# Optimization experiments

Hardware: AMD Instinct MI355X
Metric: run time of the kernel (lower is better)

The kernel has to match this reference:

```python
import jax, jax.numpy as jnp
import numpy as np

# icosphere level 6
NV = 40962   # vertices
NF = 81920   # faces
B = 16
CIN = 32
COUT = 32
NCOEFF = 4


def _spmm(rows, cols, vals, nrows, x):
    """Sparse (COO) @ dense over the vertex/face axis.
    x: [B, C, N] -> out: [B, C, nrows].
    """
    # gather columns, scale by nonzero values, scatter-add into rows
    g = x.transpose(2, 0, 1)[cols] * vals[:, None, None]   # [nnz, B, C]
    out = jax.ops.segment_sum(g, rows, num_segments=nrows)  # [nrows, B, C]
    return out.transpose(1, 2, 0)                           # [B, C, nrows]


def setup_inputs() -> dict:
    key = jax.random.key(0)
    ks = jax.random.split(key, 10)
    x = jax.random.normal(ks[0], (B, CIN, NV), dtype=jnp.float32)

    # G: [3*NF, NV], 3 nnz per row (3 vertices per face), component-major rows
    g_nnz = 3 * NF * 3
    G_rows = jnp.repeat(jnp.arange(3 * NF, dtype=jnp.int32), 3)
    G_cols = jax.random.randint(ks[1], (g_nnz,), 0, NV, dtype=jnp.int32)
    G_vals = jax.random.normal(ks[2], (g_nnz,), dtype=jnp.float32) * 0.5

    # L: [NV, NV], ~7 nnz per row (vertex valence + self)
    l_nnz = NV * 7
    L_rows = jnp.repeat(jnp.arange(NV, dtype=jnp.int32), 7)
    L_cols = jax.random.randint(ks[3], (l_nnz,), 0, NV, dtype=jnp.int32)
    L_vals = jax.random.normal(ks[4], (l_nnz,), dtype=jnp.float32) * 0.5

    # F2V: [NV, NF], ~6 faces per vertex, averaging weights
    f_nnz = NV * 6
    F2V_rows = jnp.repeat(jnp.arange(NV, dtype=jnp.int32), 6)
    F2V_cols = jax.random.randint(ks[5], (f_nnz,), 0, NF, dtype=jnp.int32)
    F2V_vals = jnp.full((f_nnz,), 1.0 / 6.0, dtype=jnp.float32)

    # per-face east-west / north-south tangent vectors: [NF, 3]
    EW = jax.random.normal(ks[6], (NF, 3), dtype=jnp.float32)
    NS = jax.random.normal(ks[7], (NF, 3), dtype=jnp.float32)

    stdv = 1.0 / np.sqrt(CIN * NCOEFF)
    coeffs = jax.random.uniform(ks[8], (COUT, CIN, NCOEFF), dtype=jnp.float32,
                                minval=-stdv, maxval=stdv)
    bias = jax.random.uniform(ks[9], (COUT,), dtype=jnp.float32,
                              minval=-stdv, maxval=stdv)

    return {
        "x": x,
        "G_rows": G_rows, "G_cols": G_cols, "G_vals": G_vals,
        "L_rows": L_rows, "L_cols": L_cols, "L_vals": L_vals,
        "F2V_rows": F2V_rows, "F2V_cols": F2V_cols, "F2V_vals": F2V_vals,
        "EW": EW, "NS": NS,
        "coeffs": coeffs, "bias": bias,
    }


def reference(x, G_rows, G_cols, G_vals, L_rows, L_cols, L_vals,
              F2V_rows, F2V_cols, F2V_vals, EW, NS, coeffs, bias):
    b, c, nv = x.shape
    # gradient on faces: [B,C,3*NF] -> [B,C,3,NF] -> [B,C,NF,3]
    grad_face = _spmm(G_rows, G_cols, G_vals, 3 * NF, x)
    grad_face = grad_face.reshape(b, c, 3, NF).transpose(0, 1, 3, 2)
    # Laplacian on vertices (stride=1 -> nv_prev = nv)
    laplacian = _spmm(L_rows, L_cols, L_vals, NV, x)
    identity = x  # x[..., :nv_prev] with nv_prev == nv
    # project face gradients onto EW / NS frames
    grad_face_ew = jnp.sum(grad_face * EW, axis=-1)  # [B,C,NF]
    grad_face_ns = jnp.sum(grad_face * NS, axis=-1)
    # average back to vertices
    grad_vert_ew = _spmm(F2V_rows, F2V_cols, F2V_vals, NV, grad_face_ew)
    grad_vert_ns = _spmm(F2V_rows, F2V_cols, F2V_vals, NV, grad_face_ns)
    # combine 4 features with learned per-channel coefficients
    feat = jnp.stack([identity, laplacian, grad_vert_ew, grad_vert_ns], axis=-1)  # [B,C,NV,4]
    out = jnp.einsum('bcnk,ock->bon', feat, coeffs) + bias[:, None]
    return out
```

## Files before the change

kernel.cpp:

```cpp
#include <hip/hip_runtime.h>
#include <hip/hip_bf16.h>

#define NVERT 40962
#define NFACE 81920
#define GRID_V ((NVERT + 3) / 4)
#define GRID_F (NFACE / 4)

typedef unsigned int uint;
typedef __attribute__((ext_vector_type(4))) uint  uintx4;
typedef __attribute__((ext_vector_type(4))) float floatx4;
typedef __attribute__((ext_vector_type(8))) short shortx8;

__device__ __forceinline__ uint packbf2(float a, float b) {
  uint ua = __float_as_uint(a); ua = ua + 0x7fffu + ((ua >> 16) & 1u);
  uint ub = __float_as_uint(b); ub = ub + 0x7fffu + ((ub >> 16) & 1u);
  return (ua >> 16) | (ub & 0xffff0000u);
}
__device__ __forceinline__ float2 unpackbf2(uint u) {
  float2 r;
  r.x = __uint_as_float(u << 16);
  r.y = __uint_as_float(u & 0xffff0000u);
  return r;
}
__device__ __forceinline__ short bfr(float x) {
  uint u = __float_as_uint(x);
  u = u + 0x7fffu + ((u >> 16) & 1u);
  return (short)(u >> 16);
}

__device__ __forceinline__ int swz(int blk, int nwg) {
  int q = nwg >> 3, r = nwg & 7;
  int xcd = blk & 7, idx = blk >> 3;
  return (xcd < r ? xcd * (q + 1) : r * (q + 1) + (xcd - r) * q) + idx;
}

__global__ __launch_bounds__(256) void k_transpose(const float* __restrict__ x,
                                                   uint* __restrict__ xT) {
  __shared__ float tile[32][33];
  int n0 = blockIdx.x * 32;
  int r0 = blockIdx.y * 32;
  int tx = threadIdx.x & 31;
  int ty = threadIdx.x >> 5;
#pragma unroll
  for (int i = 0; i < 32; i += 8) {
    int n = n0 + tx;
    tile[ty + i][tx] = (n < NVERT) ? x[(size_t)(r0 + ty + i) * NVERT + n] : 0.f;
  }
  __syncthreads();
#pragma unroll
  for (int i = 0; i < 32; i += 16) {
    int nl = (threadIdx.x >> 4) + i;
    int u  = threadIdx.x & 15;
    int n  = n0 + nl;
    int ug = 16 * blockIdx.y + u;
    int up = (ug & 3) * 64 + (ug >> 4) * 4 + ((ug >> 2) & 3);
    if (n < NVERT)
      xT[(size_t)n * 256 + up] = packbf2(tile[2 * u][nl], tile[2 * u + 1][nl]);
  }
}

__global__ __launch_bounds__(256) void k_faces(
    const uint* __restrict__ xT,
    const int* __restrict__ Gc, const float* __restrict__ Gv,
    const float* __restrict__ EW, const float* __restrict__ NS,
    uint* __restrict__ gf) {
  const int t = threadIdx.x, lane = t & 63, wid = t >> 6;
  int f = swz(blockIdx.x, GRID_F) * 4 + wid;

  float gr[3][4][2];
#pragma unroll
  for (int c = 0; c < 3; ++c)
#pragma unroll
    for (int ks = 0; ks < 4; ++ks) { gr[c][ks][0] = 0.f; gr[c][ks][1] = 0.f; }

#pragma unroll
  for (int comp = 0; comp < 3; ++comp) {
    int base = comp * (3 * NFACE) + 3 * f;
#pragma unroll
    for (int j = 0; j < 3; ++j) {
      int col = Gc[base + j];
      float v = Gv[base + j];
      uintx4 g = *(const uintx4*)(xT + (size_t)col * 256 + 4 * lane);
#pragma unroll
      for (int ks = 0; ks < 4; ++ks) {
        float2 p = unpackbf2(g[ks]);
        gr[comp][ks][0] = fmaf(v, p.x, gr[comp][ks][0]);
        gr[comp][ks][1] = fmaf(v, p.y, gr[comp][ks][1]);
      }
    }
  }
  float e0 = EW[3 * f], e1 = EW[3 * f + 1], e2 = EW[3 * f + 2];
  float s0 = NS[3 * f], s1 = NS[3 * f + 1], s2 = NS[3 * f + 2];
  uintx4 we, wn;
#pragma unroll
  for (int ks = 0; ks < 4; ++ks) {
    float ex = fmaf(e2, gr[2][ks][0], fmaf(e1, gr[1][ks][0], e0 * gr[0][ks][0]));
    float ey = fmaf(e2, gr[2][ks][1], fmaf(e1, gr[1][ks][1], e0 * gr[0][ks][1]));
    float sx = fmaf(s2, gr[2][ks][0], fmaf(s1, gr[1][ks][0], s0 * gr[0][ks][0]));
    float sy = fmaf(s2, gr[2][ks][1], fmaf(s1, gr[1][ks][1], s0 * gr[0][ks][1]));
    we[ks] = packbf2(ex, ey);
    wn[ks] = packbf2(sx, sy);
  }
  uint* op = gf + (size_t)f * 512 + 4 * lane;
  *(uintx4*)op         = we;
  *(uintx4*)(op + 256) = wn;
}

__global__ __launch_bounds__(256) void k_verts(
    const uint* __restrict__ xT,
    const int* __restrict__ Lc, const float* __restrict__ Lv,
    const int* __restrict__ Fc, const float* __restrict__ Fv,
    const uint* __restrict__ gf,
    const float* __restrict__ coeffs, const float* __restrict__ bias,
    float* __restrict__ out) {
  const int t = threadIdx.x, lane = t & 63, wid = t >> 6;
  int n = swz(blockIdx.x, GRID_V) * 4 + wid;
  if (n >= NVERT) return;
  const int h = lane >> 4, bm = lane & 15;

  uintx4 idw = *(const uintx4*)(xT + (size_t)n * 256 + 4 * lane);

  float lap[4][2], ewa[4][2], nsa[4][2];
#pragma unroll
  for (int ks = 0; ks < 4; ++ks) {
    lap[ks][0] = 0.f; lap[ks][1] = 0.f;
    ewa[ks][0] = 0.f; ewa[ks][1] = 0.f;
    nsa[ks][0] = 0.f; nsa[ks][1] = 0.f;
  }

#pragma unroll
  for (int j = 0; j < 7; ++j) {
    int col = Lc[7 * n + j];
    float v = Lv[7 * n + j];
    uintx4 g = *(const uintx4*)(xT + (size_t)col * 256 + 4 * lane);
#pragma unroll
    for (int ks = 0; ks < 4; ++ks) {
      float2 p = unpackbf2(g[ks]);
      lap[ks][0] = fmaf(v, p.x, lap[ks][0]);
      lap[ks][1] = fmaf(v, p.y, lap[ks][1]);
    }
  }
#pragma unroll
  for (int j = 0; j < 6; ++j) {
    int fc = Fc[6 * n + j];
    float v = Fv[6 * n + j];
    const uint* rp = gf + (size_t)fc * 512 + 4 * lane;
    uintx4 ge = *(const uintx4*)rp;
    uintx4 gn = *(const uintx4*)(rp + 256);
#pragma unroll
    for (int ks = 0; ks < 4; ++ks) {
      float2 a = unpackbf2(ge[ks]);
      float2 b = unpackbf2(gn[ks]);
      ewa[ks][0] = fmaf(v, a.x, ewa[ks][0]); ewa[ks][1] = fmaf(v, a.y, ewa[ks][1]);
      nsa[ks][0] = fmaf(v, b.x, nsa[ks][0]); nsa[ks][1] = fmaf(v, b.y, nsa[ks][1]);
    }
  }

  shortx8 afr[4];
#pragma unroll
  for (int ks = 0; ks < 4; ++ks) {
    float2 ip = unpackbf2(idw[ks]);
    shortx8 a;
    a[0] = bfr(ip.x);       a[1] = bfr(lap[ks][0]);
    a[2] = bfr(ewa[ks][0]); a[3] = bfr(nsa[ks][0]);
    a[4] = bfr(ip.y);       a[5] = bfr(lap[ks][1]);
    a[6] = bfr(ewa[ks][1]); a[7] = bfr(nsa[ks][1]);
    afr[ks] = a;
  }

  float b0 = bias[bm], b1 = bias[16 + bm];
  floatx4 acc0 = {b0, b0, b0, b0};
  floatx4 acc1 = {b1, b1, b1, b1};

#pragma unroll
  for (int ks = 0; ks < 4; ++ks) {
    const float* wp0 = coeffs + (size_t)bm * 128 + 32 * ks + 8 * h;
    floatx4 w0 = *(const floatx4*)wp0;
    floatx4 w1 = *(const floatx4*)(wp0 + 4);
    shortx8 bf0;
    bf0[0] = bfr(w0[0]); bf0[1] = bfr(w0[1]); bf0[2] = bfr(w0[2]); bf0[3] = bfr(w0[3]);
    bf0[4] = bfr(w1[0]); bf0[5] = bfr(w1[1]); bf0[6] = bfr(w1[2]); bf0[7] = bfr(w1[3]);
    acc0 = __builtin_amdgcn_mfma_f32_16x16x32_bf16(afr[ks], bf0, acc0, 0, 0, 0);

    const float* wp1 = wp0 + 16 * 128;
    floatx4 w2 = *(const floatx4*)wp1;
    floatx4 w3 = *(const floatx4*)(wp1 + 4);
    shortx8 bf1;
    bf1[0] = bfr(w2[0]); bf1[1] = bfr(w2[1]); bf1[2] = bfr(w2[2]); bf1[3] = bfr(w2[3]);
    bf1[4] = bfr(w3[0]); bf1[5] = bfr(w3[1]); bf1[6] = bfr(w3[2]); bf1[7] = bfr(w3[3]);
    acc1 = __builtin_amdgcn_mfma_f32_16x16x32_bf16(afr[ks], bf1, acc1, 0, 0, 0);
  }

#pragma unroll
  for (int reg = 0; reg < 4; ++reg) {
    int b = h * 4 + reg;
    out[(size_t)(b * 32 + bm) * NVERT + n]      = acc0[reg];
    out[(size_t)(b * 32 + 16 + bm) * NVERT + n] = acc1[reg];
  }
}

extern "C" void kernel_launch(void* const* d_in, const int* in_sizes, int n_in,
                              void* d_out, int out_size, void* d_ws, size_t ws_size,
                              hipStream_t stream) {
  const float* x      = (const float*)d_in[0];
  const int*   Gc     = (const int*)  d_in[2];
  const float* Gv     = (const float*)d_in[3];
  const int*   Lc     = (const int*)  d_in[5];
  const float* Lv     = (const float*)d_in[6];
  const int*   Fc     = (const int*)  d_in[8];
  const float* Fv     = (const float*)d_in[9];
  const float* EW     = (const float*)d_in[10];
  const float* NS     = (const float*)d_in[11];
  const float* coeffs = (const float*)d_in[12];
  const float* bias   = (const float*)d_in[13];
  float* out = (float*)d_out;

  uint* xT = (uint*)d_ws;
  uint* gf = xT + (size_t)NVERT * 256;

  dim3 gT((NVERT + 31) / 32, 16);
  k_transpose<<<gT, 256, 0, stream>>>(x, xT);
  k_faces<<<GRID_F, 256, 0, stream>>>(xT, Gc, Gv, EW, NS, gf);
  k_verts<<<GRID_V, 256, 0, stream>>>(xT, Lc, Lv, Fc, Fv, gf, coeffs, bias, out);
}
```

Baseline: 513.2 us.

## Fold tangent projection into face gather, precompute bf16 weights, raise occupancy

The face kernel now multiplies each gradient value by the EW/NS components as it gathers, keeping 16 accumulators instead of 24 and dropping the separate projection step. A small new kernel converts the coefficients to bf16 MFMA fragments once, so the vertex kernel loads them directly instead of converting per wave. Launch bounds now request 8 blocks per CU, and the face/vertex index is made wave-uniform with readfirstlane so index loads can be scalar. This adds one tiny kernel launch and may cause register spills under the tighter occupancy bound.

Result: slower. 978.8 us (+90.7%).

```diff
diff --git a/kernel.cpp b/kernel.cpp
--- a/kernel.cpp
+++ b/kernel.cpp
@@ -59,80 +59,91 @@
   }
 }
 
-__global__ __launch_bounds__(256) void k_faces(
+__global__ __launch_bounds__(256) void k_prepw(const float* __restrict__ coeffs,
+                                               short* __restrict__ wsW) {
+  int t = threadIdx.x;
+  int ks = t >> 6, lane = t & 63;
+  int bm = lane & 15, h = lane >> 4;
+  const float* wp0 = coeffs + (size_t)bm * 128 + 32 * ks + 8 * h;
+  shortx8 f0, f1;
+#pragma unroll
+  for (int j = 0; j < 8; ++j) {
+    f0[j] = bfr(wp0[j]);
+    f1[j] = bfr(wp0[16 * 128 + j]);
+  }
+  *(shortx8*)(wsW + ((size_t)(ks * 2 + 0) * 64 + lane) * 8) = f0;
+  *(shortx8*)(wsW + ((size_t)(ks * 2 + 1) * 64 + lane) * 8) = f1;
+}
+
+__global__ __launch_bounds__(256, 8) void k_faces(
     const uint* __restrict__ xT,
     const int* __restrict__ Gc, const float* __restrict__ Gv,
     const float* __restrict__ EW, const float* __restrict__ NS,
     uint* __restrict__ gf) {
-  const int t = threadIdx.x, lane = t & 63, wid = t >> 6;
-  int f = swz(blockIdx.x, GRID_F) * 4 + wid;
-
-  float gr[3][4][2];
-#pragma unroll
-  for (int c = 0; c < 3; ++c)
-#pragma unroll
-    for (int ks = 0; ks < 4; ++ks) { gr[c][ks][0] = 0.f; gr[c][ks][1] = 0.f; }
+  const int t = threadIdx.x, lane = t & 63;
+  const int f = __builtin_amdgcn_readfirstlane(swz(blockIdx.x, GRID_F) * 4 + (t >> 6));
+  const int voff = 4 * lane;
+
+  float ea[4][2], sa[4][2];
+#pragma unroll
+  for (int ks = 0; ks < 4; ++ks) {
+    ea[ks][0] = 0.f; ea[ks][1] = 0.f;
+    sa[ks][0] = 0.f; sa[ks][1] = 0.f;
+  }
 
 #pragma unroll
   for (int comp = 0; comp < 3; ++comp) {
-    int base = comp * (3 * NFACE) + 3 * f;
+    const int base = comp * (3 * NFACE) + 3 * f;
+    const float ewc = EW[3 * f + comp];
+    const float nsc = NS[3 * f + comp];
 #pragma unroll
     for (int j = 0; j < 3; ++j) {
-      int col = Gc[base + j];
-      float v = Gv[base + j];
-      uintx4 g = *(const uintx4*)(xT + (size_t)col * 256 + 4 * lane);
+      const int col = Gc[base + j];
+      const float v = Gv[base + j];
+      const float ve = v * ewc, vn = v * nsc;
+      uintx4 g = *(const uintx4*)(xT + (size_t)col * 256 + voff);
 #pragma unroll
       for (int ks = 0; ks < 4; ++ks) {
         float2 p = unpackbf2(g[ks]);
-        gr[comp][ks][0] = fmaf(v, p.x, gr[comp][ks][0]);
-        gr[comp][ks][1] = fmaf(v, p.y, gr[comp][ks][1]);
+        ea[ks][0] = fmaf(ve, p.x, ea[ks][0]); ea[ks][1] = fmaf(ve, p.y, ea[ks][1]);
+        sa[ks][0] = fmaf(vn, p.x, sa[ks][0]); sa[ks][1] = fmaf(vn, p.y, sa[ks][1]);
       }
     }
   }
-  float e0 = EW[3 * f], e1 = EW[3 * f + 1], e2 = EW[3 * f + 2];
-  float s0 = NS[3 * f], s1 = NS[3 * f + 1], s2 = NS[3 * f + 2];
   uintx4 we, wn;
 #pragma unroll
   for (int ks = 0; ks < 4; ++ks) {
-    float ex = fmaf(e2, gr[2][ks][0], fmaf(e1, gr[1][ks][0], e0 * gr[0][ks][0]));
-    float ey = fmaf(e2, gr[2][ks][1], fmaf(e1, gr[1][ks][1], e0 * gr[0][ks][1]));
-    float sx = fmaf(s2, gr[2][ks][0], fmaf(s1, gr[1][ks][0], s0 * gr[0][ks][0]));
-    float sy = fmaf(s2, gr[2][ks][1], fmaf(s1, gr[1][ks][1], s0 * gr[0][ks][1]));
-    we[ks] = packbf2(ex, ey);
-    wn[ks] = packbf2(sx, sy);
-  }
-  uint* op = gf + (size_t)f * 512 + 4 * lane;
+    we[ks] = packbf2(ea[ks][0], ea[ks][1]);
+    wn[ks] = packbf2(sa[ks][0], sa[ks][1]);
+  }
+  uint* op = gf + (size_t)f * 512 + voff;
   *(uintx4*)op         = we;
   *(uintx4*)(op + 256) = wn;
 }
 
-__global__ __launch_bounds__(256) void k_verts(
+__global__ __launch_bounds__(256, 8) void k_verts(
     const uint* __restrict__ xT,
     const int* __restrict__ Lc, const float* __restrict__ Lv,
     const int* __restrict__ Fc, const float* __restrict__ Fv,
     const uint* __restrict__ gf,
-    const float* __restrict__ coeffs, const float* __restrict__ bias,
+    const short* __restrict__ wsW, const float* __restrict__ bias,
     float* __restrict__ out) {
-  const int t = threadIdx.x, lane = t & 63, wid = t >> 6;
-  int n = swz(blockIdx.x, GRID_V) * 4 + wid;
+  const int t = threadIdx.x, lane = t & 63;
+  const int n = __builtin_amdgcn_readfirstlane(swz(blockIdx.x, GRID_V) * 4 + (t >> 6));
   if (n >= NVERT) return;
   const int h = lane >> 4, bm = lane & 15;
-
-  uintx4 idw = *(const uintx4*)(xT + (size_t)n * 256 + 4 * lane);
-
-  float lap[4][2], ewa[4][2], nsa[4][2];
-#pragma unroll
-  for (int ks = 0; ks < 4; ++ks) {
-    lap[ks][0] = 0.f; lap[ks][1] = 0.f;
-    ewa[ks][0] = 0.f; ewa[ks][1] = 0.f;
-    nsa[ks][0] = 0.f; nsa[ks][1] = 0.f;
-  }
-
+  const int voff = 4 * lane;
+
+  uintx4 idw = *(const uintx4*)(xT + (size_t)n * 256 + voff);
+
+  float lap[4][2];
+#pragma unroll
+  for (int ks = 0; ks < 4; ++ks) { lap[ks][0] = 0.f; lap[ks][1] = 0.f; }
 #pragma unroll
   for (int j = 0; j < 7; ++j) {
-    int col = Lc[7 * n + j];
-    float v = Lv[7 * n + j];
-    uintx4 g = *(const uintx4*)(xT + (size_t)col * 256 + 4 * lane);
+    const int col = Lc[7 * n + j];
+    const float v = Lv[7 * n + j];
+    uintx4 g = *(const uintx4*)(xT + (size_t)col * 256 + voff);
 #pragma unroll
     for (int ks = 0; ks < 4; ++ks) {
       float2 p = unpackbf2(g[ks]);
@@ -140,19 +151,26 @@
       lap[ks][1] = fmaf(v, p.y, lap[ks][1]);
     }
   }
+
+  float ea[4][2], na[4][2];
+#pragma unroll
+  for (int ks = 0; ks < 4; ++ks) {
+    ea[ks][0] = 0.f; ea[ks][1] = 0.f;
+    na[ks][0] = 0.f; na[ks][1] = 0.f;
+  }
 #pragma unroll
   for (int j = 0; j < 6; ++j) {
-    int fc = Fc[6 * n + j];
-    float v = Fv[6 * n + j];
-    const uint* rp = gf + (size_t)fc * 512 + 4 * lane;
+    const int fc = Fc[6 * n + j];
+    const float v = Fv[6 * n + j];
+    const uint* rp = gf + (size_t)fc * 512 + voff;
     uintx4 ge = *(const uintx4*)rp;
     uintx4 gn = *(const uintx4*)(rp + 256);
 #pragma unroll
     for (int ks = 0; ks < 4; ++ks) {
       float2 a = unpackbf2(ge[ks]);
       float2 b = unpackbf2(gn[ks]);
-      ewa[ks][0] = fmaf(v, a.x, ewa[ks][0]); ewa[ks][1] = fmaf(v, a.y, ewa[ks][1]);
-      nsa[ks][0] = fmaf(v, b.x, nsa[ks][0]); nsa[ks][1] = fmaf(v, b.y, nsa[ks][1]);
+      ea[ks][0] = fmaf(v, a.x, ea[ks][0]); ea[ks][1] = fmaf(v, a.y, ea[ks][1]);
+      na[ks][0] = fmaf(v, b.x, na[ks][0]); na[ks][1] = fmaf(v, b.y, na[ks][1]);
     }
   }
 
@@ -161,33 +179,21 @@
   for (int ks = 0; ks < 4; ++ks) {
     float2 ip = unpackbf2(idw[ks]);
     shortx8 a;
-    a[0] = bfr(ip.x);       a[1] = bfr(lap[ks][0]);
-    a[2] = bfr(ewa[ks][0]); a[3] = bfr(nsa[ks][0]);
-    a[4] = bfr(ip.y);       a[5] = bfr(lap[ks][1]);
-    a[6] = bfr(ewa[ks][1]); a[7] = bfr(nsa[ks][1]);
+    a[0] = bfr(ip.x);      a[1] = bfr(lap[ks][0]);
+    a[2] = bfr(ea[ks][0]); a[3] = bfr(na[ks][0]);
+    a[4] = bfr(ip.y);      a[5] = bfr(lap[ks][1]);
+    a[6] = bfr(ea[ks][1]); a[7] = bfr(na[ks][1]);
     afr[ks] = a;
   }
 
   float b0 = bias[bm], b1 = bias[16 + bm];
   floatx4 acc0 = {b0, b0, b0, b0};
   floatx4 acc1 = {b1, b1, b1, b1};
-
-#pragma unroll
-  for (int ks = 0; ks < 4; ++ks) {
-    const float* wp0 = coeffs + (size_t)bm * 128 + 32 * ks + 8 * h;
-    floatx4 w0 = *(const floatx4*)wp0;
-    floatx4 w1 = *(const floatx4*)(wp0 + 4);
-    shortx8 bf0;
-    bf0[0] = bfr(w0[0]); bf0[1] = bfr(w0[1]); bf0[2] = bfr(w0[2]); bf0[3] = bfr(w0[3]);
-    bf0[4] = bfr(w1[0]); bf0[5] = bfr(w1[1]); bf0[6] = bfr(w1[2]); bf0[7] = bfr(w1[3]);
+#pragma unroll
+  for (int ks = 0; ks < 4; ++ks) {
+    shortx8 bf0 = *(const shortx8*)(wsW + ((size_t)(ks * 2 + 0) * 64 + lane) * 8);
     acc0 = __builtin_amdgcn_mfma_f32_16x16x32_bf16(afr[ks], bf0, acc0, 0, 0, 0);
-
-    const float* wp1 = wp0 + 16 * 128;
-    floatx4 w2 = *(const floatx4*)wp1;
-    floatx4 w3 = *(const floatx4*)(wp1 + 4);
-    shortx8 bf1;
-    bf1[0] = bfr(w2[0]); bf1[1] = bfr(w2[1]); bf1[2] = bfr(w2[2]); bf1[3] = bfr(w2[3]);
-    bf1[4] = bfr(w3[0]); bf1[5] = bfr(w3[1]); bf1[6] = bfr(w3[2]); bf1[7] = bfr(w3[3]);
+    shortx8 bf1 = *(const shortx8*)(wsW + ((size_t)(ks * 2 + 1) * 64 + lane) * 8);
     acc1 = __builtin_amdgcn_mfma_f32_16x16x32_bf16(afr[ks], bf1, acc1, 0, 0, 0);
   }
 
@@ -215,11 +221,13 @@
   const float* bias   = (const float*)d_in[13];
   float* out = (float*)d_out;
 
-  uint* xT = (uint*)d_ws;
-  uint* gf = xT + (size_t)NVERT * 256;
+  uint* xT  = (uint*)d_ws;
+  uint* gf  = xT + (size_t)NVERT * 256;
+  short* wsW = (short*)(gf + (size_t)NFACE * 512);
 
   dim3 gT((NVERT + 31) / 32, 16);
   k_transpose<<<gT, 256, 0, stream>>>(x, xT);
+  k_prepw<<<1, 256, 0, stream>>>(coeffs, wsW);
   k_faces<<<GRID_F, 256, 0, stream>>>(xT, Gc, Gv, EW, NS, gf);
-  k_verts<<<GRID_V, 256, 0, stream>>>(xT, Lc, Lv, Fc, Fv, gf, coeffs, bias, out);
-}
+  k_verts<<<GRID_V, 256, 0, stream>>>(xT, Lc, Lv, Fc, Fv, gf, wsW, bias, out);
+}
```
